# Performance work log

Measured on AMD Instinct MI355X. Metric: run time of the kernel, lower is better.

Reference implementation:

```python
import jax, jax.numpy as jnp
import numpy as np

B, G, DIN, DOUT = 4096, 16, 512, 512

def setup_inputs() -> dict:
    key = jax.random.key(0)
    kx, kw, kb = jax.random.split(key, 3)
    x = jax.random.normal(kx, (B, G, DIN), dtype=jnp.float32)
    # per-group nn.Linear weight: [G, dim_out, dim_in] (torch layout)
    W = jax.random.normal(kw, (G, DOUT, DIN), dtype=jnp.float32) * (1.0 / np.sqrt(DIN))
    b = jax.random.normal(kb, (G, DOUT), dtype=jnp.float32) * 0.01
    return {"x": x, "W": W, "b": b}

def reference(x, W, b):
    # MultiLinear: independent Linear per group g; y[..., g, :] = x[..., g, :] @ W[g].T + b[g]
    # Fused as a single batched GEMM over the group dimension.
    y = jnp.einsum('bgi,goi->bgo', x, W)  # [B, G, DOUT]
    return y + b
```

## Files before the change

kernel.cpp:

```cpp
#include <hip/hip_runtime.h>
#include <hip/hip_bf16.h>


#define BATCH 4096
#define NGRP  16
#define DIN   512
#define DOUT  512

#define BM 256
#define BN 256
#define BK 64
#define NT (DIN / BK)

typedef __bf16 bf16x8 __attribute__((ext_vector_type(8)));
typedef float  f32x4  __attribute__((ext_vector_type(4)));
typedef const __attribute__((address_space(1))) void gas_void;
typedef __attribute__((address_space(3))) void las_void;

__global__ __launch_bounds__(256)
void wcvt_kernel(const float* __restrict__ W, __bf16* __restrict__ Wb) {
    const int i = (blockIdx.x * 256 + threadIdx.x) * 8;
    f32x4 a = *(const f32x4*)(W + i);
    f32x4 b = *(const f32x4*)(W + i + 4);
    bf16x8 v;
#pragma unroll
    for (int j = 0; j < 4; ++j) { v[j] = (__bf16)a[j]; v[j + 4] = (__bf16)b[j]; }
    *(bf16x8*)(Wb + i) = v;
}

__global__ __launch_bounds__(512, 2)
void MultiLinear_48498770706571_kernel(const float* __restrict__ X,
                                       const __bf16* __restrict__ Wb,
                                       const float* __restrict__ Bias,
                                       float* __restrict__ Y) {
    const int bid = (blockIdx.x & 7) * 64 + (blockIdx.x >> 3);
    const int g   = bid >> 5;
    const int mt  = (bid >> 1) & 15;
    const int nt  = bid & 1;
    const int bm0 = mt * BM;
    const int bn0 = nt * BN;

    __shared__ __bf16 As[2][BM * BK];
    __shared__ __bf16 BsF[2][BN * BK];

    const int tid  = threadIdx.x;
    const int lane = tid & 63;
    const int w    = tid >> 6;
    const int wm   = (w >> 2) * 128;
    const int wn   = (w & 3) * 64;
    const int l15  = lane & 15;
    const int q    = lane >> 4;

    const int srow = tid >> 2;
    const int sc2  = (tid & 3) * 2;
    const float* pA = X + (size_t)(bm0 + srow) * (NGRP * DIN) + g * DIN + (tid & 3) * 16;
    const size_t strideA = (size_t)128 * (NGRP * DIN);

    const int drow0 = (w << 5) + (lane >> 3);
    const int dch   = lane & 7;
    const __bf16* wbase = Wb + (size_t)g * (DOUT * DIN) + (size_t)bn0 * DIN;

    f32x4 ra[2][4];

#define ISSUE_A(k0)                                                        \
    do {                                                                   \
        const f32x4* qa0 = (const f32x4*)(pA + (k0));                      \
        const f32x4* qa1 = (const f32x4*)(pA + strideA + (k0));            \
        ra[0][0] = qa0[0]; ra[0][1] = qa0[1]; ra[0][2] = qa0[2]; ra[0][3] = qa0[3]; \
        ra[1][0] = qa1[0]; ra[1][1] = qa1[1]; ra[1][2] = qa1[2]; ra[1][3] = qa1[3]; \
    } while (0)

#define CVT_WRITE_A(buf)                                                   \
    do {                                                                   \
        _Pragma("unroll")                                                  \
        for (int p = 0; p < 2; ++p) {                                      \
            bf16x8 v0, v1;                                                 \
            _Pragma("unroll")                                              \
            for (int j = 0; j < 4; ++j) {                                  \
                v0[j] = (__bf16)ra[p][0][j]; v0[j + 4] = (__bf16)ra[p][1][j]; \
                v1[j] = (__bf16)ra[p][2][j]; v1[j + 4] = (__bf16)ra[p][3][j]; \
            }                                                              \
            const int row = p * 128 + srow;                                \
            const int s   = srow & 7;                                      \
            __bf16* base = &As[buf][row * BK];                             \
            *(bf16x8*)&base[((sc2 ^ s) << 3)]       = v0;                  \
            *(bf16x8*)&base[(((sc2 + 1) ^ s) << 3)] = v1;                  \
        }                                                                  \
    } while (0)

#define DMA_B(kt, buf)                                                     \
    do {                                                                   \
        const size_t k0 = (size_t)(kt) * BK;                               \
        _Pragma("unroll")                                                  \
        for (int qq = 0; qq < 4; ++qq) {                                   \
            const int row = drow0 + (qq << 3);                             \
            const __bf16* gp = wbase + (size_t)row * DIN + k0              \
                               + ((dch ^ (row & 7)) << 3);                 \
            __builtin_amdgcn_global_load_lds(                              \
                (gas_void*)gp,                                             \
                (las_void*)&BsF[buf][(w << 11) + (qq << 9)], 16, 0, 0);    \
        }                                                                  \
    } while (0)

#define READ_AF(MLO, KK, buf)                                              \
    do {                                                                   \
        _Pragma("unroll")                                                  \
        for (int mi = 0; mi < 4; ++mi) {                                   \
            const int row = wm + ((MLO) + mi) * 16 + l15;                  \
            const int ch  = (((KK) << 2) + q) ^ (row & 7);                 \
            af[mi] = *(const bf16x8*)&As[buf][row * BK + (ch << 3)];       \
        }                                                                  \
    } while (0)

#define READ_BF(KK, buf)                                                   \
    do {                                                                   \
        _Pragma("unroll")                                                  \
        for (int ni = 0; ni < 4; ++ni) {                                   \
            const int brow = wn + ni * 16 + l15;                           \
            const int ch   = (((KK) << 2) + q) ^ (brow & 7);               \
            bfr[ni] = *(const bf16x8*)&BsF[buf][brow * BK + (ch << 3)];    \
        }                                                                  \
    } while (0)

#define MFMA_Q(MLO)                                                        \
    do {                                                                   \
        __builtin_amdgcn_s_setprio(1);                                     \
        _Pragma("unroll")                                                  \
        for (int mi = 0; mi < 4; ++mi)                                     \
            _Pragma("unroll")                                              \
            for (int ni = 0; ni < 4; ++ni)                                 \
                acc[(MLO) + mi][ni] = __builtin_amdgcn_mfma_f32_16x16x32_bf16( \
                    af[mi], bfr[ni], acc[(MLO) + mi][ni], 0, 0, 0);        \
        __builtin_amdgcn_s_setprio(0);                                     \
    } while (0)

#define LGKM0() asm volatile("s_waitcnt lgkmcnt(0)" ::: "memory")
#define BAR()   __builtin_amdgcn_s_barrier()

    f32x4 acc[8][4];
#pragma unroll
    for (int mi = 0; mi < 8; ++mi)
#pragma unroll
        for (int ni = 0; ni < 4; ++ni) acc[mi][ni] = f32x4{0.f, 0.f, 0.f, 0.f};

    ISSUE_A(0);
    DMA_B(0, 0);
    CVT_WRITE_A(0);
    asm volatile("s_waitcnt vmcnt(0)" ::: "memory");
    LGKM0();
    BAR();

    for (int kt = 0; kt < NT; ++kt) {
        const int cur = kt & 1;
        const int nxt = cur ^ 1;
        const bool pre = (kt + 1 < NT);
        bf16x8 af[4], bfr[4];

        READ_AF(0, 0, cur);
        READ_BF(0, cur);
        if (pre) ISSUE_A((kt + 1) * BK);
        LGKM0(); BAR();
        MFMA_Q(0);
        BAR();

        READ_AF(4, 0, cur);
        if (pre) DMA_B(kt + 1, nxt);
        LGKM0(); BAR();
        MFMA_Q(4);
        BAR();

        READ_AF(0, 1, cur);
        READ_BF(1, cur);
        if (pre) CVT_WRITE_A(nxt);
        LGKM0(); BAR();
        MFMA_Q(0);
        BAR();

        READ_AF(4, 1, cur);
        LGKM0();
        if (pre) asm volatile("s_waitcnt vmcnt(0)" ::: "memory");
        BAR();
        MFMA_Q(4);
        BAR();
    }

    const int r0 = (lane >> 4) * 4;
    const int c  = lane & 15;
    float bias_n[4];
#pragma unroll
    for (int ni = 0; ni < 4; ++ni)
        bias_n[ni] = Bias[g * DOUT + bn0 + wn + ni * 16 + c];
#pragma unroll
    for (int mi = 0; mi < 8; ++mi) {
#pragma unroll
        for (int j = 0; j < 4; ++j) {
            const int row = bm0 + wm + mi * 16 + r0 + j;
            float* yrow = Y + (size_t)row * (NGRP * DOUT) + g * DOUT + bn0 + wn;
#pragma unroll
            for (int ni = 0; ni < 4; ++ni)
                yrow[ni * 16 + c] = acc[mi][ni][j] + bias_n[ni];
        }
    }
#undef ISSUE_A
#undef CVT_WRITE_A
#undef DMA_B
#undef READ_AF
#undef READ_BF
#undef MFMA_Q
#undef LGKM0
#undef BAR
}

extern "C" void kernel_launch(void* const* d_in, const int* in_sizes, int n_in,
                              void* d_out, int out_size, void* d_ws, size_t ws_size,
                              hipStream_t stream) {
    const float* X    = (const float*)d_in[0];
    const float* W    = (const float*)d_in[1];
    const float* Bias = (const float*)d_in[2];
    float* Y          = (float*)d_out;
    __bf16* Wb        = (__bf16*)d_ws;

    wcvt_kernel<<<2048, 256, 0, stream>>>(W, Wb);

    const int grid = NGRP * (BATCH / BM) * (DOUT / BN);
    MultiLinear_48498770706571_kernel<<<grid, 512, 0, stream>>>(X, Wb, Bias, Y);
}
```

Before: 89.82 us.

## Retile to 128x512 blocks so each fp32 X tile is converted once

Block tile changes from 256x256 to 128x512, so each workgroup covers the full output width of a group. Each fp32 X row is then loaded and converted to bf16 by one block only, where before two blocks per M-tile did this. The B DMA is split into two halves issued in separate phases, and the vmcnt wait moves to the top of the next iteration, which changes how loads overlap with compute. LDS use and B traffic per block go up, and all 8 waves now share the same A rows.

```diff
diff --git a/kernel.cpp b/kernel.cpp
--- a/kernel.cpp
+++ b/kernel.cpp
@@ -7,8 +7,8 @@
 #define DIN   512
 #define DOUT  512
 
-#define BM 256
-#define BN 256
+#define BM 128
+#define BN 512
 #define BK 64
 #define NT (DIN / BK)
 
@@ -35,10 +35,8 @@
                                        float* __restrict__ Y) {
     const int bid = (blockIdx.x & 7) * 64 + (blockIdx.x >> 3);
     const int g   = bid >> 5;
-    const int mt  = (bid >> 1) & 15;
-    const int nt  = bid & 1;
+    const int mt  = bid & 31;
     const int bm0 = mt * BM;
-    const int bn0 = nt * BN;
 
     __shared__ __bf16 As[2][BM * BK];
     __shared__ __bf16 BsF[2][BN * BK];
@@ -46,59 +44,51 @@
     const int tid  = threadIdx.x;
     const int lane = tid & 63;
     const int w    = tid >> 6;
-    const int wm   = (w >> 2) * 128;
-    const int wn   = (w & 3) * 64;
+    const int wn   = w * 64;
     const int l15  = lane & 15;
     const int q    = lane >> 4;
 
     const int srow = tid >> 2;
     const int sc2  = (tid & 3) * 2;
     const float* pA = X + (size_t)(bm0 + srow) * (NGRP * DIN) + g * DIN + (tid & 3) * 16;
-    const size_t strideA = (size_t)128 * (NGRP * DIN);
-
-    const int drow0 = (w << 5) + (lane >> 3);
-    const int dch   = lane & 7;
-    const __bf16* wbase = Wb + (size_t)g * (DOUT * DIN) + (size_t)bn0 * DIN;
-
-    f32x4 ra[2][4];
+
+    const int drow_l = lane >> 3;
+    const int dch    = lane & 7;
+    const __bf16* wbase = Wb + (size_t)g * (DOUT * DIN);
+
+    f32x4 ra[4];
 
 #define ISSUE_A(k0)                                                        \
     do {                                                                   \
-        const f32x4* qa0 = (const f32x4*)(pA + (k0));                      \
-        const f32x4* qa1 = (const f32x4*)(pA + strideA + (k0));            \
-        ra[0][0] = qa0[0]; ra[0][1] = qa0[1]; ra[0][2] = qa0[2]; ra[0][3] = qa0[3]; \
-        ra[1][0] = qa1[0]; ra[1][1] = qa1[1]; ra[1][2] = qa1[2]; ra[1][3] = qa1[3]; \
+        const f32x4* qa = (const f32x4*)(pA + (k0));                       \
+        ra[0] = qa[0]; ra[1] = qa[1]; ra[2] = qa[2]; ra[3] = qa[3];        \
     } while (0)
 
 #define CVT_WRITE_A(buf)                                                   \
     do {                                                                   \
-        _Pragma("unroll")                                                  \
-        for (int p = 0; p < 2; ++p) {                                      \
-            bf16x8 v0, v1;                                                 \
-            _Pragma("unroll")                                              \
-            for (int j = 0; j < 4; ++j) {                                  \
-                v0[j] = (__bf16)ra[p][0][j]; v0[j + 4] = (__bf16)ra[p][1][j]; \
-                v1[j] = (__bf16)ra[p][2][j]; v1[j + 4] = (__bf16)ra[p][3][j]; \
-            }                                                              \
-            const int row = p * 128 + srow;                                \
-            const int s   = srow & 7;                                      \
-            __bf16* base = &As[buf][row * BK];                             \
-            *(bf16x8*)&base[((sc2 ^ s) << 3)]       = v0;                  \
-            *(bf16x8*)&base[(((sc2 + 1) ^ s) << 3)] = v1;                  \
-        }                                                                  \
-    } while (0)
-
-#define DMA_B(kt, buf)                                                     \
+        bf16x8 v0, v1;                                                     \
+        _Pragma("unroll")                                                  \
+        for (int j = 0; j < 4; ++j) {                                      \
+            v0[j] = (__bf16)ra[0][j]; v0[j + 4] = (__bf16)ra[1][j];        \
+            v1[j] = (__bf16)ra[2][j]; v1[j + 4] = (__bf16)ra[3][j];        \
+        }                                                                  \
+        const int s = srow & 7;                                            \
+        __bf16* base = &As[buf][srow * BK];                                \
+        *(bf16x8*)&base[((sc2 ^ s) << 3)]       = v0;                      \
+        *(bf16x8*)&base[(((sc2 + 1) ^ s) << 3)] = v1;                      \
+    } while (0)
+
+#define DMA_B_HALF(kt, buf, H)                                             \
     do {                                                                   \
         const size_t k0 = (size_t)(kt) * BK;                               \
         _Pragma("unroll")                                                  \
-        for (int qq = 0; qq < 4; ++qq) {                                   \
-            const int row = drow0 + (qq << 3);                             \
+        for (int qq = (H) * 4; qq < (H) * 4 + 4; ++qq) {                   \
+            const int row = (w << 6) + (qq << 3) + drow_l;                 \
             const __bf16* gp = wbase + (size_t)row * DIN + k0              \
                                + ((dch ^ (row & 7)) << 3);                 \
             __builtin_amdgcn_global_load_lds(                              \
                 (gas_void*)gp,                                             \
-                (las_void*)&BsF[buf][(w << 11) + (qq << 9)], 16, 0, 0);    \
+                (las_void*)&BsF[buf][(w << 12) + (qq << 9)], 16, 0, 0);    \
         }                                                                  \
     } while (0)
 
@@ -106,7 +96,7 @@
     do {                                                                   \
         _Pragma("unroll")                                                  \
         for (int mi = 0; mi < 4; ++mi) {                                   \
-            const int row = wm + ((MLO) + mi) * 16 + l15;                  \
+            const int row = ((MLO) + mi) * 16 + l15;                       \
             const int ch  = (((KK) << 2) + q) ^ (row & 7);                 \
             af[mi] = *(const bf16x8*)&As[buf][row * BK + (ch << 3)];       \
         }                                                                  \
@@ -144,11 +134,9 @@
         for (int ni = 0; ni < 4; ++ni) acc[mi][ni] = f32x4{0.f, 0.f, 0.f, 0.f};
 
     ISSUE_A(0);
-    DMA_B(0, 0);
+    DMA_B_HALF(0, 0, 0);
+    DMA_B_HALF(0, 0, 1);
     CVT_WRITE_A(0);
-    asm volatile("s_waitcnt vmcnt(0)" ::: "memory");
-    LGKM0();
-    BAR();
 
     for (int kt = 0; kt < NT; ++kt) {
         const int cur = kt & 1;
@@ -156,15 +144,24 @@
         const bool pre = (kt + 1 < NT);
         bf16x8 af[4], bfr[4];
 
+        if (pre) {
+            ISSUE_A((kt + 1) * BK);
+            asm volatile("s_waitcnt vmcnt(4)" ::: "memory");
+        } else {
+            asm volatile("s_waitcnt vmcnt(0)" ::: "memory");
+        }
+        LGKM0();
+        BAR();
+
         READ_AF(0, 0, cur);
         READ_BF(0, cur);
-        if (pre) ISSUE_A((kt + 1) * BK);
+        if (pre) DMA_B_HALF(kt + 1, nxt, 0);
         LGKM0(); BAR();
         MFMA_Q(0);
         BAR();
 
         READ_AF(4, 0, cur);
-        if (pre) DMA_B(kt + 1, nxt);
+        if (pre) DMA_B_HALF(kt + 1, nxt, 1);
         LGKM0(); BAR();
         MFMA_Q(4);
         BAR();
@@ -177,9 +174,7 @@
         BAR();
 
         READ_AF(4, 1, cur);
-        LGKM0();
-        if (pre) asm volatile("s_waitcnt vmcnt(0)" ::: "memory");
-        BAR();
+        LGKM0(); BAR();
         MFMA_Q(4);
         BAR();
     }
@@ -189,13 +184,13 @@
     float bias_n[4];
 #pragma unroll
     for (int ni = 0; ni < 4; ++ni)
-        bias_n[ni] = Bias[g * DOUT + bn0 + wn + ni * 16 + c];
+        bias_n[ni] = Bias[g * DOUT + wn + ni * 16 + c];
 #pragma unroll
     for (int mi = 0; mi < 8; ++mi) {
 #pragma unroll
         for (int j = 0; j < 4; ++j) {
-            const int row = bm0 + wm + mi * 16 + r0 + j;
-            float* yrow = Y + (size_t)row * (NGRP * DOUT) + g * DOUT + bn0 + wn;
+            const int row = bm0 + mi * 16 + r0 + j;
+            float* yrow = Y + (size_t)row * (NGRP * DOUT) + g * DOUT + wn;
 #pragma unroll
             for (int ni = 0; ni < 4; ++ni)
                 yrow[ni * 16 + c] = acc[mi][ni][j] + bias_n[ni];
@@ -203,7 +198,7 @@
     }
 #undef ISSUE_A
 #undef CVT_WRITE_A
-#undef DMA_B
+#undef DMA_B_HALF
 #undef READ_AF
 #undef READ_BF
 #undef MFMA_Q
@@ -222,6 +217,6 @@
 
     wcvt_kernel<<<2048, 256, 0, stream>>>(W, Wb);
 
-    const int grid = NGRP * (BATCH / BM) * (DOUT / BN);
+    const int grid = NGRP * (BATCH / BM);
     MultiLinear_48498770706571_kernel<<<grid, 512, 0, stream>>>(X, Wb, Bias, Y);
 }
```

Measured after the change: 79.72 us. 11.3% less time.
